# Kernel tuning notes

Measured on AMD Instinct MI355X. Metric: run time of the kernel, lower is better.

## Reference

```python
import jax, jax.numpy as jnp
import numpy as np

D_MODEL = 3072
N_HEADS = 24
MAX_LEN = 2048
ROPE_THETA = 10000.0
DH = D_MODEL // N_HEADS                  # 128
Q_PROJ = D_MODEL // 2                    # 1536
KV_PROJ = 2 * D_MODEL // 3               # 2048
NOPE = DH // 2                           # 64
ROPE = DH // 2                           # 64
EPS = 1e-5


def layernorm(x, w, b):
    m = jnp.mean(x, axis=-1, keepdims=True)
    v = jnp.mean(jnp.square(x - m), axis=-1, keepdims=True)
    return (x - m) / jnp.sqrt(v + EPS) * w + b


def rotate_half(x):
    h = x.shape[-1] // 2
    return jnp.concatenate([-x[..., h:], x[..., :h]], axis=-1)


def rope_tables(S):
    freqs = 1.0 / ROPE_THETA ** (jnp.arange(0, DH, 2, dtype=jnp.float32) / DH)  # [DH/2]
    emb = jnp.arange(S, dtype=jnp.float32)[:, None] * freqs[None, :]            # [S, DH/2]
    # torch: take first ROPE//2 freqs then .repeat(...,2) => tile along last axis
    cos = jnp.tile(jnp.cos(emb)[:, : ROPE // 2], (1, 2))  # [S, ROPE]
    sin = jnp.tile(jnp.sin(emb)[:, : ROPE // 2], (1, 2))
    return cos[None, None], sin[None, None]               # [1,1,S,ROPE]


def setup_inputs() -> dict:
    key = jax.random.key(0)
    ks = jax.random.split(key, 7)
    x = jax.random.normal(ks[0], (2, 2048, D_MODEL), dtype=jnp.float32)
    p = lambda k, shp: 0.01 * jax.random.normal(k, shp, dtype=jnp.float32)
    return {
        "x": x,
        "W_dq": p(ks[1], (D_MODEL, Q_PROJ)),
        "W_uq": p(ks[2], (Q_PROJ, D_MODEL)),
        "q_ln_w": jnp.ones((Q_PROJ,), jnp.float32),
        "q_ln_b": jnp.zeros((Q_PROJ,), jnp.float32),
        "W_dkv": p(ks[3], (D_MODEL, KV_PROJ + ROPE)),
        "W_ukv": p(ks[4], (KV_PROJ, D_MODEL + N_HEADS * NOPE)),
        "kv_ln_w": jnp.ones((KV_PROJ,), jnp.float32),
        "kv_ln_b": jnp.zeros((KV_PROJ,), jnp.float32),
        "W_o": p(ks[5], (D_MODEL, D_MODEL)),
    }


def reference(x, W_dq, W_uq, q_ln_w, q_ln_b, W_dkv, W_ukv, kv_ln_w, kv_ln_b, W_o):
    B, S, D = x.shape
    cos, sin = rope_tables(S)  # past_length=0, S_full=S

    # Q path: low-rank down/up projection
    cq = layernorm(x @ W_dq, q_ln_w, q_ln_b)          # [B,S,Q_PROJ]
    Q = (cq @ W_uq).reshape(B, S, N_HEADS, DH).transpose(0, 2, 1, 3)  # [B,H,S,DH]
    Q_nope, Q_rope = Q[..., :NOPE], Q[..., NOPE:]
    Q_rope = Q_rope * cos + rotate_half(Q_rope) * sin

    # KV path
    compressed_kv = x @ W_dkv                          # [B,S,KV_PROJ+ROPE]
    KV_lora = layernorm(compressed_kv[..., :KV_PROJ], kv_ln_w, kv_ln_b)
    K_rope = compressed_kv[..., KV_PROJ:]              # [B,S,ROPE]
    KV = (KV_lora @ W_ukv).reshape(B, S, N_HEADS, DH + NOPE).transpose(0, 2, 1, 3)
    K_nope, V = KV[..., :NOPE], KV[..., NOPE:]         # [B,H,S,NOPE], [B,H,S,DH]

    K_rope = K_rope[:, None]                           # [B,1,S,ROPE] shared head
    K_rope = K_rope * cos + rotate_half(K_rope) * sin

    q = jnp.concatenate([Q_nope, Q_rope], axis=-1)     # [B,H,S,DH]
    # k = cat(K_nope, K_rope broadcast over heads)
    k = jnp.concatenate([K_nope, jnp.broadcast_to(K_rope, (B, N_HEADS, S, ROPE))], axis=-1)

    scale = 1.0 / jnp.sqrt(jnp.float32(DH))
    scores = jnp.einsum("bhqd,bhkd->bhqk", q, k) * scale
    causal = jnp.tril(jnp.ones((S, S), dtype=bool))
    scores = jnp.where(causal[None, None], scores, jnp.float32(-jnp.inf))
    attn = jax.nn.softmax(scores, axis=-1)
    out = jnp.einsum("bhqk,bhkd->bhqd", attn, V)
    out = out.transpose(0, 2, 1, 3).reshape(B, S, D)
    out = out @ W_o.T
    return out, compressed_kv
```

## Files before the change

kernel.cpp:

```cpp
#include <hip/hip_runtime.h>

typedef unsigned short u16;
typedef __attribute__((ext_vector_type(8))) short short8;
typedef __attribute__((ext_vector_type(4))) float f32x4;

#define NROWS   4096
#define S_LEN   2048
#define NHEADS  24
#define DMODEL  3072
#define QPROJ   1536
#define KVPROJ  2048
#define CKV_W   2112
#define UKV_N   4608

__device__ __forceinline__ float bf2f(u16 v) {
    unsigned u = ((unsigned)v) << 16; float f; __builtin_memcpy(&f, &u, 4); return f;
}
__device__ __forceinline__ u16 f2bf(float f) {
    unsigned u; __builtin_memcpy(&u, &f, 4);
    u = (u + 0x7FFFu + ((u >> 16) & 1u)) >> 16; return (u16)u;
}
__device__ __forceinline__ void async16(const u16* g, u16* l) {
    __builtin_amdgcn_global_load_lds((const __attribute__((address_space(1))) unsigned int*)g,
                                     (__attribute__((address_space(3))) unsigned int*)l,
                                     16, 0, 0);
}

__global__ void conv_bf16(const float* __restrict__ X, u16* __restrict__ Y, int n) {
    int i = (blockIdx.x * 256 + threadIdx.x) * 4;
    if (i >= n) return;
    float4 v = *(const float4*)(X + i);
    Y[i+0] = f2bf(v.x); Y[i+1] = f2bf(v.y); Y[i+2] = f2bf(v.z); Y[i+3] = f2bf(v.w);
}

__global__ void transpose_bf16(const float* __restrict__ W, u16* __restrict__ WT,
                               int K, int N, float scale) {
    __shared__ float t[32][33];
    int nb = blockIdx.x * 32, kb = blockIdx.y * 32;
    int c = threadIdx.x & 31, rq = threadIdx.x >> 5;
#pragma unroll
    for (int i = 0; i < 4; ++i) {
        int r = rq * 4 + i;
        t[r][c] = W[(size_t)(kb + r) * N + nb + c];
    }
    __syncthreads();
#pragma unroll
    for (int i = 0; i < 4; ++i) {
        int r = rq * 4 + i;
        WT[(size_t)(nb + r) * K + kb + c] = f2bf(t[c][r] * scale);
    }
}

__global__ __launch_bounds__(256) void ln_kernel(const float* __restrict__ X, int ldx,
                                                 const float* __restrict__ g,
                                                 const float* __restrict__ b,
                                                 u16* __restrict__ Y, int W) {
    int row = blockIdx.x;
    const float* x = X + (size_t)row * ldx;
    float s = 0.f, s2 = 0.f;
    for (int i = threadIdx.x; i < W; i += 256) { float v = x[i]; s += v; s2 += v * v; }
#pragma unroll
    for (int off = 32; off >= 1; off >>= 1) { s += __shfl_xor(s, off); s2 += __shfl_xor(s2, off); }
    __shared__ float red[8];
    int w = threadIdx.x >> 6;
    if ((threadIdx.x & 63) == 0) { red[w] = s; red[4 + w] = s2; }
    __syncthreads();
    s  = red[0] + red[1] + red[2] + red[3];
    s2 = red[4] + red[5] + red[6] + red[7];
    float mean = s / W;
    float var  = s2 / W - mean * mean;
    float rstd = rsqrtf(var + 1e-5f);
    u16* y = Y + (size_t)row * W;
    for (int i = threadIdx.x; i < W; i += 256)
        y[i] = f2bf((x[i] - mean) * rstd * g[i] + b[i]);
}

__global__ void rope_q_kernel(u16* __restrict__ Q) {
    int idx = blockIdx.x * 256 + threadIdx.x;
    int j = idx & 31; int t = idx >> 5; int h = t % NHEADS; int row = t / NHEADS;
    int s = row & (S_LEN - 1);
    float freq = __expf(-(float)j * (9.210340371976184f / 64.f));
    float ang = (float)s * freq;
    float c = cosf(ang), si = sinf(ang);
    u16* p = Q + (size_t)row * DMODEL + h * 128 + 64;
    float x1 = bf2f(p[j]), x2 = bf2f(p[j + 32]);
    p[j]      = f2bf(x1 * c - x2 * si);
    p[j + 32] = f2bf(x2 * c + x1 * si);
}

__global__ void rope_k_kernel(const float* __restrict__ ckv, u16* __restrict__ kr) {
    int idx = blockIdx.x * 256 + threadIdx.x;
    int j = idx & 31; int row = idx >> 5;
    int s = row & (S_LEN - 1);
    float freq = __expf(-(float)j * (9.210340371976184f / 64.f));
    float ang = (float)s * freq;
    float c = cosf(ang), si = sinf(ang);
    const float* src = ckv + (size_t)row * CKV_W + KVPROJ;
    float x1 = src[j], x2 = src[j + 32];
    kr[(size_t)row * 64 + j]      = f2bf(x1 * c - x2 * si);
    kr[(size_t)row * 64 + j + 32] = f2bf(x2 * c + x1 * si);
}

__global__ __launch_bounds__(256) void pack_k(const u16* __restrict__ KVb,
                                              const u16* __restrict__ kr,
                                              u16* __restrict__ Kp) {
    int bh = blockIdx.y, bb = bh / NHEADS, h = bh % NHEADS;
    int s0 = blockIdx.x * 64;
    int t = threadIdx.x;
    size_t base = (size_t)bb * S_LEN;
#pragma unroll
    for (int it = 0; it < 4; ++it) {
        int j = it * 256 + t;
        int r = j >> 4, cb = (j & 15) * 8;
        int s = s0 + r;
        uint4 v;
        if (cb < 64) v = *(const uint4*)&KVb[(base + s) * UKV_N + h * 192 + cb];
        else         v = *(const uint4*)&kr[(base + s) * 64 + (cb - 64)];
        *(uint4*)&Kp[((size_t)bh * S_LEN + s) * 128 + cb] = v;
    }
}

__global__ __launch_bounds__(256) void pack_v(const u16* __restrict__ KVb,
                                              u16* __restrict__ Vt) {
    __shared__ u16 tile[64][136];
    int bh = blockIdx.y, bb = bh / NHEADS, h = bh % NHEADS;
    int s0 = blockIdx.x * 64;
    int t = threadIdx.x;
    size_t base = (size_t)bb * S_LEN;
#pragma unroll
    for (int it = 0; it < 4; ++it) {
        int j = it * 256 + t;
        int r = j >> 4, cb = (j & 15) * 8;
        *(uint4*)&tile[r][cb] = *(const uint4*)&KVb[(base + s0 + r) * UKV_N + h * 192 + 64 + cb];
    }
    __syncthreads();
#pragma unroll
    for (int it = 0; it < 4; ++it) {
        int j = it * 256 + t;
        int d = j >> 3, sb = (j & 7) * 8;
        u16 tmp[8];
#pragma unroll
        for (int e = 0; e < 8; ++e) tmp[e] = tile[sb + e][d];
        *(uint4*)&Vt[((size_t)bh * 128 + d) * S_LEN + s0 + sb] = *(uint4*)tmp;
    }
}

template<bool OUT_BF16>
__global__ __launch_bounds__(256) void gemm_nt(const u16* __restrict__ A,
                                               const u16* __restrict__ B,
                                               void* __restrict__ Cv,
                                               int M, int N, int K) {
    __shared__ u16 a_lds[2][128][32];
    __shared__ u16 b_lds[2][128][32];
    int m0 = blockIdx.y * 128, n0 = blockIdx.x * 128;
    int tid = threadIdx.x, lane = tid & 63, w = tid >> 6;
    int wm = w >> 1, wn = w & 1;
    int srow = lane >> 2;
    int kx = (lane >> 4) & 2;
    int scol = ((lane & 3) ^ kx) * 8;
    int r0 = w * 32 + srow, r1 = w * 32 + 16 + srow;
    const u16* A0 = A + (size_t)(m0 + r0) * K + scol;
    const u16* A1 = A + (size_t)(m0 + r1) * K + scol;
    int bn0 = n0 + r0; if (bn0 >= N) bn0 = N - 1;
    int bn1 = n0 + r1; if (bn1 >= N) bn1 = N - 1;
    const u16* B0 = B + (size_t)bn0 * K + scol;
    const u16* B1 = B + (size_t)bn1 * K + scol;
    char* aB = (char*)&a_lds[0][0][0];
    char* bB = (char*)&b_lds[0][0][0];
    int d0 = w * 2048, d1 = w * 2048 + 1024;
    int cb = ((lane >> 4) * 16) ^ ((lane & 8) << 2);

    f32x4 acc[4][4] = {};
    async16(A0, (u16*)(aB + d0)); async16(A1, (u16*)(aB + d1));
    async16(B0, (u16*)(bB + d0)); async16(B1, (u16*)(bB + d1));
    __syncthreads();
    int buf = 0;
    for (int kb = 0; kb < K; kb += 32) {
        if (kb + 32 < K) {
            int ob = (buf ^ 1) * 8192;
            async16(A0 + kb + 32, (u16*)(aB + ob + d0));
            async16(A1 + kb + 32, (u16*)(aB + ob + d1));
            async16(B0 + kb + 32, (u16*)(bB + ob + d0));
            async16(B1 + kb + 32, (u16*)(bB + ob + d1));
        }
        const char* ab = aB + buf * 8192;
        const char* bb = bB + buf * 8192;
        short8 af[4], bf[4];
#pragma unroll
        for (int i = 0; i < 4; ++i) {
            af[i] = *(const short8*)(ab + (wm * 64 + i * 16 + (lane & 15)) * 64 + cb);
            bf[i] = *(const short8*)(bb + (wn * 64 + i * 16 + (lane & 15)) * 64 + cb);
        }
#pragma unroll
        for (int i = 0; i < 4; ++i)
#pragma unroll
            for (int j = 0; j < 4; ++j)
                acc[i][j] = __builtin_amdgcn_mfma_f32_16x16x32_bf16(af[i], bf[j], acc[i][j], 0, 0, 0);
        __syncthreads();
        buf ^= 1;
    }
#pragma unroll
    for (int i = 0; i < 4; ++i) {
        int row = m0 + wm * 64 + i * 16 + ((lane >> 4) << 2);
#pragma unroll
        for (int j = 0; j < 4; ++j) {
            int col = n0 + wn * 64 + j * 16 + (lane & 15);
            if (col < N) {
#pragma unroll
                for (int r = 0; r < 4; ++r) {
                    if (OUT_BF16) ((u16*)Cv)[(size_t)(row + r) * N + col] = f2bf(acc[i][j][r]);
                    else          ((float*)Cv)[(size_t)(row + r) * N + col] = acc[i][j][r];
                }
            }
        }
    }
}

__global__ __launch_bounds__(256) void attn_kernel(const u16* __restrict__ Qb,
                                                   const u16* __restrict__ Kp,
                                                   const u16* __restrict__ Vt,
                                                   u16* __restrict__ AO) {
    __shared__ u16 k_lds[64][128];
    __shared__ u16 v_lds[128][64];
    __shared__ u16 p_lds[4][16][72];
    int bid = blockIdx.x;
    int jj = bid >> 3;
    int bh = (bid & 7) * 6 + (jj >> 4);
    int bx = jj & 15;
    int bb = bh / NHEADS, h = bh % NHEADS;
    int tid = threadIdx.x, lane = tid & 63, w = tid >> 6;
    size_t base = (size_t)bb * S_LEN;
    size_t bhS = (size_t)bh * S_LEN;

    const char* Kbyte = (const char*)Kp;
    const char* Vbyte = (const char*)Vt;
    char* kB = (char*)&k_lds[0][0];
    char* vB = (char*)&v_lds[0][0];
    size_t ksrc[4], vsrc[4];
    int kd[4];
#pragma unroll
    for (int is = 0; is < 4; ++is) {
        int j = is * 256 + tid;
        int r = j >> 4;
        int cbs = ((j & 15) * 16) ^ ((r & 7) << 4);
        ksrc[is] = (bhS + r) * 256 + cbs;
        int d = j >> 3;
        int kbs = (((j & 7) ^ (d & 7)) * 16);
        vsrc[is] = ((size_t)bh * 128 + d) * (S_LEN * 2) + kbs;
        kd[is] = (is * 256 + w * 64) * 16;
    }

    for (int seg = 0; seg < 2; ++seg) {
        int qx = seg == 0 ? (31 - bx) : bx;
        int q0 = qx * 64;

        short8 qf[4];
        {
            int qrow = q0 + w * 16 + (lane & 15);
            const u16* qp = Qb + (base + qrow) * DMODEL + h * 128 + ((lane >> 4) * 8);
#pragma unroll
            for (int ks = 0; ks < 4; ++ks) qf[ks] = *(const short8*)(qp + ks * 32);
        }

        f32x4 acc_o[8] = {};
        float m_run[4], l_run[4];
#pragma unroll
        for (int r = 0; r < 4; ++r) { m_run[r] = -1e30f; l_run[r] = 0.f; }

        int ntiles = qx + 1;
        for (int t = 0; t < ntiles; ++t) {
            size_t kv0 = (size_t)t * 64;
#pragma unroll
            for (int is = 0; is < 4; ++is)
                async16((const u16*)(Kbyte + ksrc[is] + kv0 * 256), (u16*)(kB + kd[is]));
#pragma unroll
            for (int is = 0; is < 4; ++is)
                async16((const u16*)(Vbyte + vsrc[is] + kv0 * 2), (u16*)(vB + kd[is]));
            __syncthreads();

            f32x4 sc[4];
            __builtin_amdgcn_s_setprio(1);
#pragma unroll
            for (int nb = 0; nb < 4; ++nb) {
                f32x4 a = {};
                int row = nb * 16 + (lane & 15);
                const char* kb_ = kB + row * 256;
                int x = (row & 7) << 4;
#pragma unroll
                for (int ks = 0; ks < 4; ++ks) {
                    short8 kf = *(const short8*)(kb_ + ((ks * 64 + (lane >> 4) * 16) ^ x));
                    a = __builtin_amdgcn_mfma_f32_16x16x32_bf16(qf[ks], kf, a, 0, 0, 0);
                }
                sc[nb] = a;
            }
            __builtin_amdgcn_s_setprio(0);

            if (t == qx) {
                int kvb = t * 64;
                int qg = q0 + w * 16 + ((lane >> 4) << 2);
#pragma unroll
                for (int nb = 0; nb < 4; ++nb) {
                    int kc = kvb + nb * 16 + (lane & 15);
#pragma unroll
                    for (int r = 0; r < 4; ++r)
                        if (kc > qg + r) sc[nb][r] = -1e30f;
                }
            }
            float rmax[4];
#pragma unroll
            for (int r = 0; r < 4; ++r)
                rmax[r] = fmaxf(fmaxf(sc[0][r], sc[1][r]), fmaxf(sc[2][r], sc[3][r]));
#pragma unroll
            for (int off = 1; off < 16; off <<= 1)
#pragma unroll
                for (int r = 0; r < 4; ++r) rmax[r] = fmaxf(rmax[r], __shfl_xor(rmax[r], off));

            bool ok = (rmax[0] <= m_run[0]) & (rmax[1] <= m_run[1]) &
                      (rmax[2] <= m_run[2]) & (rmax[3] <= m_run[3]);
            if (!__all(ok)) {
                float fac[4];
#pragma unroll
                for (int r = 0; r < 4; ++r) {
                    float mnew = fmaxf(m_run[r], rmax[r]);
                    fac[r] = __expf(m_run[r] - mnew);
                    m_run[r] = mnew;
                    l_run[r] *= fac[r];
                }
#pragma unroll
                for (int db = 0; db < 8; ++db)
#pragma unroll
                    for (int r = 0; r < 4; ++r) acc_o[db][r] *= fac[r];
            }
            float rsum[4] = {0.f, 0.f, 0.f, 0.f};
#pragma unroll
            for (int nb = 0; nb < 4; ++nb)
#pragma unroll
                for (int r = 0; r < 4; ++r) {
                    float p = __expf(sc[nb][r] - m_run[r]);
                    sc[nb][r] = p; rsum[r] += p;
                }
#pragma unroll
            for (int off = 1; off < 16; off <<= 1)
#pragma unroll
                for (int r = 0; r < 4; ++r) rsum[r] += __shfl_xor(rsum[r], off);
#pragma unroll
            for (int r = 0; r < 4; ++r) l_run[r] += rsum[r];

#pragma unroll
            for (int nb = 0; nb < 4; ++nb)
#pragma unroll
                for (int r = 0; r < 4; ++r)
                    p_lds[w][((lane >> 4) << 2) + r][nb * 16 + (lane & 15)] = f2bf(sc[nb][r]);
            __builtin_amdgcn_sched_barrier(0);
            __builtin_amdgcn_s_setprio(1);
#pragma unroll
            for (int ks = 0; ks < 2; ++ks) {
                short8 pf = *(const short8*)&p_lds[w][lane & 15][ks * 32 + (lane >> 4) * 8];
#pragma unroll
                for (int db = 0; db < 8; ++db) {
                    int row = db * 16 + (lane & 15);
                    const char* vb_ = vB + row * 128;
                    short8 vf = *(const short8*)(vb_ + ((ks * 64 + (lane >> 4) * 16) ^ ((row & 7) << 4)));
                    acc_o[db] = __builtin_amdgcn_mfma_f32_16x16x32_bf16(pf, vf, acc_o[db], 0, 0, 0);
                }
            }
            __builtin_amdgcn_s_setprio(0);
            __syncthreads();
        }

        int orow = q0 + w * 16 + ((lane >> 4) << 2);
#pragma unroll
        for (int db = 0; db < 8; ++db)
#pragma unroll
            for (int r = 0; r < 4; ++r) {
                float o = acc_o[db][r] / l_run[r];
                AO[(base + orow + r) * DMODEL + h * 128 + db * 16 + (lane & 15)] = f2bf(o);
            }
    }
}

extern "C" void kernel_launch(void* const* d_in, const int* in_sizes, int n_in,
                              void* d_out, int out_size, void* d_ws, size_t ws_size,
                              hipStream_t stream) {
    (void)in_sizes; (void)n_in; (void)out_size; (void)ws_size;
    const float* x      = (const float*)d_in[0];
    const float* W_dq   = (const float*)d_in[1];
    const float* W_uq   = (const float*)d_in[2];
    const float* q_ln_w = (const float*)d_in[3];
    const float* q_ln_b = (const float*)d_in[4];
    const float* W_dkv  = (const float*)d_in[5];
    const float* W_ukv  = (const float*)d_in[6];
    const float* kv_ln_w= (const float*)d_in[7];
    const float* kv_ln_b= (const float*)d_in[8];
    const float* W_o    = (const float*)d_in[9];

    float* out = (float*)d_out;
    float* ckv = out + (size_t)NROWS * DMODEL;

    char* ws = (char*)d_ws;
    const size_t OFF_WDQT  = 0;
    const size_t OFF_WUQT  = 9437184;
    const size_t OFF_WDKVT = 18874368;
    const size_t OFF_WUKVT = 31850496;
    const size_t OFF_WO    = 50724864;
    const size_t OFF_XB    = 69599232;
    const size_t OFF_QB    = 94765056;
    const size_t OFF_KVB   = 119930880;
    const size_t OFF_KR    = 157679616;
    const size_t OFF_SLABA = 158203904;
    const size_t OFF_SLABB = 183369728;
    const size_t OFF_KP    = 0;
    const size_t OFF_VT    = OFF_XB;

    u16* Wdq_t  = (u16*)(ws + OFF_WDQT);
    u16* Wuq_t  = (u16*)(ws + OFF_WUQT);
    u16* Wdkv_t = (u16*)(ws + OFF_WDKVT);
    u16* Wukv_t = (u16*)(ws + OFF_WUKVT);
    u16* Wo_b   = (u16*)(ws + OFF_WO);
    u16* xb     = (u16*)(ws + OFF_XB);
    u16* qb     = (u16*)(ws + OFF_QB);
    u16* KVb    = (u16*)(ws + OFF_KVB);
    u16* kr     = (u16*)(ws + OFF_KR);
    float* t0   = (float*)(ws + OFF_SLABA);
    u16* ao     = (u16*)(ws + OFF_SLABA);
    u16* cq     = (u16*)(ws + OFF_SLABB);
    u16* kvl    = (u16*)(ws + OFF_SLABB);
    u16* Kp     = (u16*)(ws + OFF_KP);
    u16* Vt     = (u16*)(ws + OFF_VT);

    const float SCALE = 0.08838834764831845f;

    transpose_bf16<<<dim3(QPROJ / 32, DMODEL / 32), 256, 0, stream>>>(W_dq,  Wdq_t,  DMODEL, QPROJ, 1.0f);
    transpose_bf16<<<dim3(DMODEL / 32, QPROJ / 32), 256, 0, stream>>>(W_uq,  Wuq_t,  QPROJ, DMODEL, SCALE);
    transpose_bf16<<<dim3(CKV_W / 32, DMODEL / 32), 256, 0, stream>>>(W_dkv, Wdkv_t, DMODEL, CKV_W, 1.0f);
    transpose_bf16<<<dim3(UKV_N / 32, KVPROJ / 32), 256, 0, stream>>>(W_ukv, Wukv_t, KVPROJ, UKV_N, 1.0f);
    conv_bf16<<<9216, 256, 0, stream>>>(W_o, Wo_b, DMODEL * DMODEL);
    conv_bf16<<<12288, 256, 0, stream>>>(x, xb, NROWS * DMODEL);

    gemm_nt<false><<<dim3(QPROJ / 128, NROWS / 128), 256, 0, stream>>>(xb, Wdq_t, t0, NROWS, QPROJ, DMODEL);
    ln_kernel<<<NROWS, 256, 0, stream>>>(t0, QPROJ, q_ln_w, q_ln_b, cq, QPROJ);
    gemm_nt<true><<<dim3(DMODEL / 128, NROWS / 128), 256, 0, stream>>>(cq, Wuq_t, qb, NROWS, DMODEL, QPROJ);
    rope_q_kernel<<<12288, 256, 0, stream>>>(qb);

    gemm_nt<false><<<dim3((CKV_W + 127) / 128, NROWS / 128), 256, 0, stream>>>(xb, Wdkv_t, ckv, NROWS, CKV_W, DMODEL);
    ln_kernel<<<NROWS, 256, 0, stream>>>(ckv, CKV_W, kv_ln_w, kv_ln_b, kvl, KVPROJ);
    rope_k_kernel<<<512, 256, 0, stream>>>(ckv, kr);
    gemm_nt<true><<<dim3(UKV_N / 128, NROWS / 128), 256, 0, stream>>>(kvl, Wukv_t, KVb, NROWS, UKV_N, KVPROJ);

    pack_k<<<dim3(S_LEN / 64, 2 * NHEADS), 256, 0, stream>>>(KVb, kr, Kp);
    pack_v<<<dim3(S_LEN / 64, 2 * NHEADS), 256, 0, stream>>>(KVb, Vt);

    attn_kernel<<<768, 256, 0, stream>>>(qb, Kp, Vt, ao);

    gemm_nt<false><<<dim3(DMODEL / 128, NROWS / 128), 256, 0, stream>>>(ao, Wo_b, out, NROWS, DMODEL, DMODEL);
}
```

Measured before the change: 672.4 us.

## Add 256x256-tile GEMM for large projections and defer softmax row-sum reduction

New measurement: 676.0 us. No clear change (+0.5%).

```diff
diff --git a/kernel.cpp b/kernel.cpp
--- a/kernel.cpp
+++ b/kernel.cpp
@@ -216,6 +216,99 @@
     }
 }
 
+template<bool OUT_BF16>
+__global__ __launch_bounds__(512) void gemm_nt256(const u16* __restrict__ A,
+                                                  const u16* __restrict__ B,
+                                                  void* __restrict__ Cv,
+                                                  int M, int N, int K) {
+    __shared__ u16 a_lds[2][256][64];
+    __shared__ u16 b_lds[2][256][64];
+    int m0 = blockIdx.y * 256, n0 = blockIdx.x * 256;
+    int tid = threadIdx.x, lane = tid & 63, w = tid >> 6;
+    int wm = w >> 2, wn = w & 3;
+
+    const u16* As[4]; const u16* Bs[4]; int dst[4];
+#pragma unroll
+    for (int is = 0; is < 4; ++is) {
+        int g = is * 512 + tid;
+        int row = g >> 3;
+        int sc = ((g & 7) ^ (row & 7)) * 8;
+        As[is] = A + (size_t)(m0 + row) * K + sc;
+        Bs[is] = B + (size_t)(n0 + row) * K + sc;
+        dst[is] = (is * 512 + w * 64) * 16;
+    }
+    char* aB = (char*)&a_lds[0][0][0];
+    char* bB = (char*)&b_lds[0][0][0];
+
+    f32x4 acc[8][4] = {};
+#pragma unroll
+    for (int is = 0; is < 4; ++is) {
+        async16(As[is], (u16*)(aB + dst[is]));
+        async16(Bs[is], (u16*)(bB + dst[is]));
+    }
+    __syncthreads();
+    int buf = 0;
+    for (int kb = 0; kb < K; kb += 64) {
+        if (kb + 64 < K) {
+            int ob = (buf ^ 1) * 32768;
+#pragma unroll
+            for (int is = 0; is < 4; ++is) {
+                async16(As[is] + kb + 64, (u16*)(aB + ob + dst[is]));
+                async16(Bs[is] + kb + 64, (u16*)(bB + ob + dst[is]));
+            }
+        }
+        const char* ab = aB + buf * 32768;
+        const char* bb = bB + buf * 32768;
+#pragma unroll
+        for (int mh = 0; mh < 2; ++mh) {
+            short8 af[4][2];
+#pragma unroll
+            for (int i = 0; i < 4; ++i)
+#pragma unroll
+                for (int kh = 0; kh < 2; ++kh) {
+                    int row = wm * 128 + mh * 64 + i * 16 + (lane & 15);
+                    int cbb = (kh * 64 + ((lane >> 4) * 16)) ^ ((row & 7) << 4);
+                    af[i][kh] = *(const short8*)(ab + row * 128 + cbb);
+                }
+#pragma unroll
+            for (int nh = 0; nh < 2; ++nh) {
+                short8 bf[2][2];
+#pragma unroll
+                for (int j = 0; j < 2; ++j)
+#pragma unroll
+                    for (int kh = 0; kh < 2; ++kh) {
+                        int row = wn * 64 + nh * 32 + j * 16 + (lane & 15);
+                        int cbb = (kh * 64 + ((lane >> 4) * 16)) ^ ((row & 7) << 4);
+                        bf[j][kh] = *(const short8*)(bb + row * 128 + cbb);
+                    }
+#pragma unroll
+                for (int i = 0; i < 4; ++i)
+#pragma unroll
+                    for (int j = 0; j < 2; ++j)
+#pragma unroll
+                        for (int kh = 0; kh < 2; ++kh)
+                            acc[mh * 4 + i][nh * 2 + j] = __builtin_amdgcn_mfma_f32_16x16x32_bf16(
+                                af[i][kh], bf[j][kh], acc[mh * 4 + i][nh * 2 + j], 0, 0, 0);
+            }
+        }
+        __syncthreads();
+        buf ^= 1;
+    }
+#pragma unroll
+    for (int mf = 0; mf < 8; ++mf) {
+        int row = m0 + wm * 128 + mf * 16 + ((lane >> 4) << 2);
+#pragma unroll
+        for (int nf = 0; nf < 4; ++nf) {
+            int col = n0 + wn * 64 + nf * 16 + (lane & 15);
+#pragma unroll
+            for (int r = 0; r < 4; ++r) {
+                if (OUT_BF16) ((u16*)Cv)[(size_t)(row + r) * N + col] = f2bf(acc[mf][nf][r]);
+                else          ((float*)Cv)[(size_t)(row + r) * N + col] = acc[mf][nf][r];
+            }
+        }
+    }
+}
+
 __global__ __launch_bounds__(256) void attn_kernel(const u16* __restrict__ Qb,
                                                    const u16* __restrict__ Kp,
                                                    const u16* __restrict__ Vt,
@@ -331,20 +424,13 @@
 #pragma unroll
                     for (int r = 0; r < 4; ++r) acc_o[db][r] *= fac[r];
             }
-            float rsum[4] = {0.f, 0.f, 0.f, 0.f};
 #pragma unroll
             for (int nb = 0; nb < 4; ++nb)
 #pragma unroll
                 for (int r = 0; r < 4; ++r) {
                     float p = __expf(sc[nb][r] - m_run[r]);
-                    sc[nb][r] = p; rsum[r] += p;
-                }
-#pragma unroll
-            for (int off = 1; off < 16; off <<= 1)
-#pragma unroll
-                for (int r = 0; r < 4; ++r) rsum[r] += __shfl_xor(rsum[r], off);
-#pragma unroll
-            for (int r = 0; r < 4; ++r) l_run[r] += rsum[r];
+                    sc[nb][r] = p; l_run[r] += p;
+                }
 
 #pragma unroll
             for (int nb = 0; nb < 4; ++nb)
@@ -367,6 +453,11 @@
             __builtin_amdgcn_s_setprio(0);
             __syncthreads();
         }
+
+#pragma unroll
+        for (int off = 1; off < 16; off <<= 1)
+#pragma unroll
+            for (int r = 0; r < 4; ++r) l_run[r] += __shfl_xor(l_run[r], off);
 
         int orow = q0 + w * 16 + ((lane >> 4) << 2);
 #pragma unroll
@@ -439,18 +530,18 @@
 
     gemm_nt<false><<<dim3(QPROJ / 128, NROWS / 128), 256, 0, stream>>>(xb, Wdq_t, t0, NROWS, QPROJ, DMODEL);
     ln_kernel<<<NROWS, 256, 0, stream>>>(t0, QPROJ, q_ln_w, q_ln_b, cq, QPROJ);
-    gemm_nt<true><<<dim3(DMODEL / 128, NROWS / 128), 256, 0, stream>>>(cq, Wuq_t, qb, NROWS, DMODEL, QPROJ);
+    gemm_nt256<true><<<dim3(DMODEL / 256, NROWS / 256), 512, 0, stream>>>(cq, Wuq_t, qb, NROWS, DMODEL, QPROJ);
     rope_q_kernel<<<12288, 256, 0, stream>>>(qb);
 
     gemm_nt<false><<<dim3((CKV_W + 127) / 128, NROWS / 128), 256, 0, stream>>>(xb, Wdkv_t, ckv, NROWS, CKV_W, DMODEL);
     ln_kernel<<<NROWS, 256, 0, stream>>>(ckv, CKV_W, kv_ln_w, kv_ln_b, kvl, KVPROJ);
     rope_k_kernel<<<512, 256, 0, stream>>>(ckv, kr);
-    gemm_nt<true><<<dim3(UKV_N / 128, NROWS / 128), 256, 0, stream>>>(kvl, Wukv_t, KVb, NROWS, UKV_N, KVPROJ);
+    gemm_nt256<true><<<dim3(UKV_N / 256, NROWS / 256), 512, 0, stream>>>(kvl, Wukv_t, KVb, NROWS, UKV_N, KVPROJ);
 
     pack_k<<<dim3(S_LEN / 64, 2 * NHEADS), 256, 0, stream>>>(KVb, kr, Kp);
     pack_v<<<dim3(S_LEN / 64, 2 * NHEADS), 256, 0, stream>>>(KVb, Vt);
 
     attn_kernel<<<768, 256, 0, stream>>>(qb, Kp, Vt, ao);
 
-    gemm_nt<false><<<dim3(DMODEL / 128, NROWS / 128), 256, 0, stream>>>(ao, Wo_b, out, NROWS, DMODEL, DMODEL);
-}
+    gemm_nt256<false><<<dim3(DMODEL / 256, NROWS / 256), 512, 0, stream>>>(ao, Wo_b, out, NROWS, DMODEL, DMODEL);
+}
```

## Process 128 query rows per attention block with two 16-row tiles per wave

Applied to the files above, without the earlier changes.

Result: slower. 737.7 us (+9.7%).

```diff
diff --git a/kernel.cpp b/kernel.cpp
--- a/kernel.cpp
+++ b/kernel.cpp
@@ -222,11 +222,11 @@
                                                    u16* __restrict__ AO) {
     __shared__ u16 k_lds[64][128];
     __shared__ u16 v_lds[128][64];
-    __shared__ u16 p_lds[4][16][72];
+    __shared__ u16 p_lds[4][32][72];
     int bid = blockIdx.x;
     int jj = bid >> 3;
-    int bh = (bid & 7) * 6 + (jj >> 4);
-    int bx = jj & 15;
+    int bh = (bid & 7) * 6 + (jj >> 3);
+    int pr = jj & 7;
     int bb = bh / NHEADS, h = bh % NHEADS;
     int tid = threadIdx.x, lane = tid & 63, w = tid >> 6;
     size_t base = (size_t)bb * S_LEN;
@@ -251,23 +251,29 @@
     }
 
     for (int seg = 0; seg < 2; ++seg) {
-        int qx = seg == 0 ? (31 - bx) : bx;
-        int q0 = qx * 64;
-
-        short8 qf[4];
+        int qx = seg == 0 ? (15 - pr) : pr;
+        int q0 = qx * 128;
+
+        short8 qf0[4], qf1[4];
         {
-            int qrow = q0 + w * 16 + (lane & 15);
-            const u16* qp = Qb + (base + qrow) * DMODEL + h * 128 + ((lane >> 4) * 8);
-#pragma unroll
-            for (int ks = 0; ks < 4; ++ks) qf[ks] = *(const short8*)(qp + ks * 32);
+            int qrow = q0 + w * 32 + (lane & 15);
+            const u16* qp0 = Qb + (base + qrow) * DMODEL + h * 128 + ((lane >> 4) * 8);
+            const u16* qp1 = qp0 + 16 * DMODEL;
+#pragma unroll
+            for (int ks = 0; ks < 4; ++ks) {
+                qf0[ks] = *(const short8*)(qp0 + ks * 32);
+                qf1[ks] = *(const short8*)(qp1 + ks * 32);
+            }
         }
 
-        f32x4 acc_o[8] = {};
-        float m_run[4], l_run[4];
-#pragma unroll
-        for (int r = 0; r < 4; ++r) { m_run[r] = -1e30f; l_run[r] = 0.f; }
-
-        int ntiles = qx + 1;
+        f32x4 acc0[8] = {}, acc1[8] = {};
+        float m0[4], l0[4], m1[4], l1[4];
+#pragma unroll
+        for (int r = 0; r < 4; ++r) { m0[r] = -1e30f; l0[r] = 0.f; m1[r] = -1e30f; l1[r] = 0.f; }
+
+        int ntiles = 2 * qx + 2;
+        int wave_nt = ((q0 + w * 32 + 31) >> 6) + 1;
+
         for (int t = 0; t < ntiles; ++t) {
             size_t kv0 = (size_t)t * 64;
 #pragma unroll
@@ -278,103 +284,117 @@
                 async16((const u16*)(Vbyte + vsrc[is] + kv0 * 2), (u16*)(vB + kd[is]));
             __syncthreads();
 
-            f32x4 sc[4];
-            __builtin_amdgcn_s_setprio(1);
-#pragma unroll
-            for (int nb = 0; nb < 4; ++nb) {
-                f32x4 a = {};
-                int row = nb * 16 + (lane & 15);
-                const char* kb_ = kB + row * 256;
-                int x = (row & 7) << 4;
-#pragma unroll
-                for (int ks = 0; ks < 4; ++ks) {
-                    short8 kf = *(const short8*)(kb_ + ((ks * 64 + (lane >> 4) * 16) ^ x));
-                    a = __builtin_amdgcn_mfma_f32_16x16x32_bf16(qf[ks], kf, a, 0, 0, 0);
-                }
-                sc[nb] = a;
+            if (t < wave_nt) {
+                f32x4 sc0[4], sc1[4];
+                __builtin_amdgcn_s_setprio(1);
+#pragma unroll
+                for (int nb = 0; nb < 4; ++nb) {
+                    f32x4 a0 = {}, a1 = {};
+                    int row = nb * 16 + (lane & 15);
+                    const char* kb_ = kB + row * 256;
+                    int x = (row & 7) << 4;
+#pragma unroll
+                    for (int ks = 0; ks < 4; ++ks) {
+                        short8 kf = *(const short8*)(kb_ + ((ks * 64 + (lane >> 4) * 16) ^ x));
+                        a0 = __builtin_amdgcn_mfma_f32_16x16x32_bf16(qf0[ks], kf, a0, 0, 0, 0);
+                        a1 = __builtin_amdgcn_mfma_f32_16x16x32_bf16(qf1[ks], kf, a1, 0, 0, 0);
+                    }
+                    sc0[nb] = a0; sc1[nb] = a1;
+                }
+                __builtin_amdgcn_s_setprio(0);
+
+                if (t + 1 == wave_nt) {
+                    int kvb = t * 64;
+                    int qg0 = q0 + w * 32 + ((lane >> 4) << 2);
+                    int qg1 = qg0 + 16;
+#pragma unroll
+                    for (int nb = 0; nb < 4; ++nb) {
+                        int kc = kvb + nb * 16 + (lane & 15);
+#pragma unroll
+                        for (int r = 0; r < 4; ++r) {
+                            if (kc > qg0 + r) sc0[nb][r] = -1e30f;
+                            if (kc > qg1 + r) sc1[nb][r] = -1e30f;
+                        }
+                    }
+                }
+                float rx0[4], rx1[4];
+#pragma unroll
+                for (int r = 0; r < 4; ++r) {
+                    rx0[r] = fmaxf(fmaxf(sc0[0][r], sc0[1][r]), fmaxf(sc0[2][r], sc0[3][r]));
+                    rx1[r] = fmaxf(fmaxf(sc1[0][r], sc1[1][r]), fmaxf(sc1[2][r], sc1[3][r]));
+                }
+#pragma unroll
+                for (int off = 1; off < 16; off <<= 1)
+#pragma unroll
+                    for (int r = 0; r < 4; ++r) {
+                        rx0[r] = fmaxf(rx0[r], __shfl_xor(rx0[r], off));
+                        rx1[r] = fmaxf(rx1[r], __shfl_xor(rx1[r], off));
+                    }
+
+                bool ok = (rx0[0] <= m0[0]) & (rx0[1] <= m0[1]) & (rx0[2] <= m0[2]) & (rx0[3] <= m0[3]) &
+                          (rx1[0] <= m1[0]) & (rx1[1] <= m1[1]) & (rx1[2] <= m1[2]) & (rx1[3] <= m1[3]);
+                if (!__all(ok)) {
+                    float f0[4], f1[4];
+#pragma unroll
+                    for (int r = 0; r < 4; ++r) {
+                        float n0_ = fmaxf(m0[r], rx0[r]); f0[r] = __expf(m0[r] - n0_); m0[r] = n0_; l0[r] *= f0[r];
+                        float n1_ = fmaxf(m1[r], rx1[r]); f1[r] = __expf(m1[r] - n1_); m1[r] = n1_; l1[r] *= f1[r];
+                    }
+#pragma unroll
+                    for (int db = 0; db < 8; ++db)
+#pragma unroll
+                        for (int r = 0; r < 4; ++r) { acc0[db][r] *= f0[r]; acc1[db][r] *= f1[r]; }
+                }
+#pragma unroll
+                for (int nb = 0; nb < 4; ++nb)
+#pragma unroll
+                    for (int r = 0; r < 4; ++r) {
+                        float p0 = __expf(sc0[nb][r] - m0[r]); sc0[nb][r] = p0; l0[r] += p0;
+                        float p1 = __expf(sc1[nb][r] - m1[r]); sc1[nb][r] = p1; l1[r] += p1;
+                    }
+
+#pragma unroll
+                for (int nb = 0; nb < 4; ++nb)
+#pragma unroll
+                    for (int r = 0; r < 4; ++r) {
+                        p_lds[w][((lane >> 4) << 2) + r][nb * 16 + (lane & 15)] = f2bf(sc0[nb][r]);
+                        p_lds[w][16 + ((lane >> 4) << 2) + r][nb * 16 + (lane & 15)] = f2bf(sc1[nb][r]);
+                    }
+                __builtin_amdgcn_sched_barrier(0);
+                __builtin_amdgcn_s_setprio(1);
+#pragma unroll
+                for (int ks = 0; ks < 2; ++ks) {
+                    short8 pf0 = *(const short8*)&p_lds[w][lane & 15][ks * 32 + (lane >> 4) * 8];
+                    short8 pf1 = *(const short8*)&p_lds[w][16 + (lane & 15)][ks * 32 + (lane >> 4) * 8];
+#pragma unroll
+                    for (int db = 0; db < 8; ++db) {
+                        int row = db * 16 + (lane & 15);
+                        const char* vb_ = vB + row * 128;
+                        short8 vf = *(const short8*)(vb_ + ((ks * 64 + (lane >> 4) * 16) ^ ((row & 7) << 4)));
+                        acc0[db] = __builtin_amdgcn_mfma_f32_16x16x32_bf16(pf0, vf, acc0[db], 0, 0, 0);
+                        acc1[db] = __builtin_amdgcn_mfma_f32_16x16x32_bf16(pf1, vf, acc1[db], 0, 0, 0);
+                    }
+                }
+                __builtin_amdgcn_s_setprio(0);
             }
-            __builtin_amdgcn_s_setprio(0);
-
-            if (t == qx) {
-                int kvb = t * 64;
-                int qg = q0 + w * 16 + ((lane >> 4) << 2);
-#pragma unroll
-                for (int nb = 0; nb < 4; ++nb) {
-                    int kc = kvb + nb * 16 + (lane & 15);
-#pragma unroll
-                    for (int r = 0; r < 4; ++r)
-                        if (kc > qg + r) sc[nb][r] = -1e30f;
-                }
-            }
-            float rmax[4];
-#pragma unroll
-            for (int r = 0; r < 4; ++r)
-                rmax[r] = fmaxf(fmaxf(sc[0][r], sc[1][r]), fmaxf(sc[2][r], sc[3][r]));
-#pragma unroll
-            for (int off = 1; off < 16; off <<= 1)
-#pragma unroll
-                for (int r = 0; r < 4; ++r) rmax[r] = fmaxf(rmax[r], __shfl_xor(rmax[r], off));
-
-            bool ok = (rmax[0] <= m_run[0]) & (rmax[1] <= m_run[1]) &
-                      (rmax[2] <= m_run[2]) & (rmax[3] <= m_run[3]);
-            if (!__all(ok)) {
-                float fac[4];
-#pragma unroll
-                for (int r = 0; r < 4; ++r) {
-                    float mnew = fmaxf(m_run[r], rmax[r]);
-                    fac[r] = __expf(m_run[r] - mnew);
-                    m_run[r] = mnew;
-                    l_run[r] *= fac[r];
-                }
-#pragma unroll
-                for (int db = 0; db < 8; ++db)
-#pragma unroll
-                    for (int r = 0; r < 4; ++r) acc_o[db][r] *= fac[r];
-            }
-            float rsum[4] = {0.f, 0.f, 0.f, 0.f};
-#pragma unroll
-            for (int nb = 0; nb < 4; ++nb)
-#pragma unroll
-                for (int r = 0; r < 4; ++r) {
-                    float p = __expf(sc[nb][r] - m_run[r]);
-                    sc[nb][r] = p; rsum[r] += p;
-                }
-#pragma unroll
-            for (int off = 1; off < 16; off <<= 1)
-#pragma unroll
-                for (int r = 0; r < 4; ++r) rsum[r] += __shfl_xor(rsum[r], off);
-#pragma unroll
-            for (int r = 0; r < 4; ++r) l_run[r] += rsum[r];
-
-#pragma unroll
-            for (int nb = 0; nb < 4; ++nb)
-#pragma unroll
-                for (int r = 0; r < 4; ++r)
-                    p_lds[w][((lane >> 4) << 2) + r][nb * 16 + (lane & 15)] = f2bf(sc[nb][r]);
-            __builtin_amdgcn_sched_barrier(0);
-            __builtin_amdgcn_s_setprio(1);
-#pragma unroll
-            for (int ks = 0; ks < 2; ++ks) {
-                short8 pf = *(const short8*)&p_lds[w][lane & 15][ks * 32 + (lane >> 4) * 8];
-#pragma unroll
-                for (int db = 0; db < 8; ++db) {
-                    int row = db * 16 + (lane & 15);
-                    const char* vb_ = vB + row * 128;
-                    short8 vf = *(const short8*)(vb_ + ((ks * 64 + (lane >> 4) * 16) ^ ((row & 7) << 4)));
-                    acc_o[db] = __builtin_amdgcn_mfma_f32_16x16x32_bf16(pf, vf, acc_o[db], 0, 0, 0);
-                }
-            }
-            __builtin_amdgcn_s_setprio(0);
             __syncthreads();
         }
 
-        int orow = q0 + w * 16 + ((lane >> 4) << 2);
+#pragma unroll
+        for (int off = 1; off < 16; off <<= 1)
+#pragma unroll
+            for (int r = 0; r < 4; ++r) {
+                l0[r] += __shfl_xor(l0[r], off);
+                l1[r] += __shfl_xor(l1[r], off);
+            }
+
+        int orow0 = q0 + w * 32 + ((lane >> 4) << 2);
 #pragma unroll
         for (int db = 0; db < 8; ++db)
 #pragma unroll
             for (int r = 0; r < 4; ++r) {
-                float o = acc_o[db][r] / l_run[r];
-                AO[(base + orow + r) * DMODEL + h * 128 + db * 16 + (lane & 15)] = f2bf(o);
+                AO[(base + orow0 + r) * DMODEL + h * 128 + db * 16 + (lane & 15)] = f2bf(acc0[db][r] / l0[r]);
+                AO[(base + orow0 + 16 + r) * DMODEL + h * 128 + db * 16 + (lane & 15)] = f2bf(acc1[db][r] / l1[r]);
             }
     }
 }
@@ -450,7 +470,7 @@
     pack_k<<<dim3(S_LEN / 64, 2 * NHEADS), 256, 0, stream>>>(KVb, kr, Kp);
     pack_v<<<dim3(S_LEN / 64, 2 * NHEADS), 256, 0, stream>>>(KVb, Vt);
 
-    attn_kernel<<<768, 256, 0, stream>>>(qb, Kp, Vt, ao);
+    attn_kernel<<<384, 256, 0, stream>>>(qb, Kp, Vt, ao);
 
     gemm_nt<false><<<dim3(DMODEL / 128, NROWS / 128), 256, 0, stream>>>(ao, Wo_b, out, NROWS, DMODEL, DMODEL);
 }
```
